# Kernel tuning notes

Hardware: AMD Instinct MI355X
Metric: run time of the kernel (lower is better)

Reference implementation:

```python
import jax, jax.numpy as jnp
import numpy as np

B, S, E, H = 2, 2048, 1024, 16
D = E // H  # head_dim = 64
SCALE = 1.0 / np.sqrt(D)


def setup_inputs() -> dict:
    key = jax.random.key(0)
    ks = jax.random.split(key, 5)
    std = 0.02
    return {
        "x": jax.random.normal(ks[0], (B, S, E), dtype=jnp.float32),
        "wq": jax.random.normal(ks[1], (E, E), dtype=jnp.float32) * std,
        "wk": jax.random.normal(ks[2], (E, E), dtype=jnp.float32) * std,
        "wv": jax.random.normal(ks[3], (E, E), dtype=jnp.float32) * std,
        "wo": jax.random.normal(ks[4], (E, E), dtype=jnp.float32) * std,
    }


def reference(x, wq, wk, wv, wo):
    # Linear projections (torch Linear: y = x @ W.T); weights stored as [out, in]
    q = jnp.einsum('bse,fe->bsf', x, wq)
    k = jnp.einsum('bse,fe->bsf', x, wk)
    v = jnp.einsum('bse,fe->bsf', x, wv)
    # split heads -> [B, H, S, D]
    q = q.reshape(B, S, H, D).transpose(0, 2, 1, 3)
    k = k.reshape(B, S, H, D).transpose(0, 2, 1, 3)
    v = v.reshape(B, S, H, D).transpose(0, 2, 1, 3)
    # scaled dot-product scores [B, H, S, S]
    scores = jnp.einsum('bhqd,bhkd->bhqk', q, k) * SCALE
    # causal mask: -inf above diagonal
    causal = jnp.triu(jnp.full((S, S), -jnp.inf, dtype=scores.dtype), k=1)
    scores = scores + causal[None, None, :, :]
    attn = jax.nn.softmax(scores, axis=-1)
    # dropout p=0 -> identity
    out = jnp.einsum('bhqk,bhkd->bhqd', attn, v)
    out = out.transpose(0, 2, 1, 3).reshape(B, S, E)
    return jnp.einsum('bse,fe->bsf', out, wo)
```

## Files before the change

kernel.cpp:

```cpp
#include <hip/hip_runtime.h>
#include <hip/hip_bf16.h>

#define B_ 2
#define S_ 2048
#define E_ 1024
#define H_ 16
#define D_ 64
#define QKV_N 3072
#define C2_ 0.18033688011112042f

typedef __attribute__((ext_vector_type(8))) unsigned short ushort8_t;
typedef __attribute__((ext_vector_type(8))) short short8_t;
typedef __attribute__((ext_vector_type(4))) float f32x4;

__device__ __forceinline__ unsigned short f2b(float f) {
    union { float f; unsigned u; } x; x.f = f;
    unsigned r = x.u + 0x7FFFu + ((x.u >> 16) & 1u);
    return (unsigned short)(r >> 16);
}
__device__ __forceinline__ ushort2 pkbf(float a, float b) {
    union { __hip_bfloat162 h; ushort2 u; } c;
    c.h = __float22bfloat162_rn(make_float2(a, b));
    return c.u;
}
__device__ __forceinline__ void glds16(const unsigned short* g, unsigned short* l) {
    __builtin_amdgcn_global_load_lds((const __attribute__((address_space(1))) void*)g,
                                     (__attribute__((address_space(3))) void*)l, 16, 0, 0);
}

__global__ __launch_bounds__(256) void cast_all(const float* __restrict__ x,
                                                const float* __restrict__ wq,
                                                const float* __restrict__ wk,
                                                const float* __restrict__ wv,
                                                const float* __restrict__ wo,
                                                unsigned short* __restrict__ xb,
                                                unsigned short* __restrict__ wb) {
    int idx = blockIdx.x * 256 + threadIdx.x;
    const float* src; unsigned short* dst; float s = 1.f; int j;
    if (idx < 1048576) {
        src = x; dst = xb; j = idx;
    } else {
        j = idx - 1048576;
        int y = j >> 18;
        src = (y == 0) ? wq : (y == 1) ? wk : (y == 2) ? wv : wo;
        dst = wb + (size_t)y * 1048576;
        j &= 262143;
        if (y == 0) s = C2_;
    }
    float4 v = ((const float4*)src)[j];
    ushort2 lo = pkbf(v.x * s, v.y * s), hi = pkbf(v.z * s, v.w * s);
    ((ushort4*)dst)[j] = make_ushort4(lo.x, lo.y, hi.x, hi.y);
}

template <int TM, bool OUT_BF16>
__device__ __forceinline__ void gemm_bt_body(const unsigned short* __restrict__ A,
                                             const unsigned short* __restrict__ Bt,
                                             void* __restrict__ Cout,
                                             int N, int K) {
    __shared__ unsigned short As[TM * 32];
    __shared__ unsigned short Bs[128 * 32];
    const int m0 = blockIdx.y * TM;
    const int n0 = blockIdx.x * 128;
    const int tid = threadIdx.x;
    const int wave = tid >> 6;
    const int lane = tid & 63;
    const int wm = (wave >> 1) * (TM / 2);
    const int wn = (wave & 1) * 64;
    const int quad = lane >> 4;
    const int l15 = lane & 15;
    constexpr int MI = TM / 32;

    f32x4 acc[MI][4] = {};

    const int srow = lane >> 2;
    const int scb  = (lane & 3) * 8;
    const unsigned short* gB0 = Bt + (size_t)(n0 + wave * 32 + srow) * K + scb;
    const unsigned short* gB1 = gB0 + (size_t)16 * K;
    unsigned short* lB0 = Bs + wave * 1024;
    unsigned short* lB1 = lB0 + 512;
    const unsigned short* gA0;
    const unsigned short* gA1 = nullptr;
    unsigned short* lA0;
    unsigned short* lA1 = nullptr;
    if (TM == 128) {
        gA0 = A + (size_t)(m0 + wave * 32 + srow) * K + scb;
        gA1 = gA0 + (size_t)16 * K;
        lA0 = As + wave * 1024; lA1 = lA0 + 512;
    } else {
        gA0 = A + (size_t)(m0 + wave * 16 + srow) * K + scb;
        lA0 = As + wave * 512;
    }

    for (int k0 = 0; k0 < K; k0 += 32) {
        __syncthreads();
        glds16(gA0 + k0, lA0);
        if (TM == 128) glds16(gA1 + k0, lA1);
        glds16(gB0 + k0, lB0);
        glds16(gB1 + k0, lB1);
        __syncthreads();

        short8_t af[MI], bfv[4];
#pragma unroll
        for (int mi = 0; mi < MI; ++mi)
            af[mi] = *(const short8_t*)(&As[(wm + mi * 16 + l15) * 32 + quad * 8]);
#pragma unroll
        for (int ni = 0; ni < 4; ++ni)
            bfv[ni] = *(const short8_t*)(&Bs[(wn + ni * 16 + l15) * 32 + quad * 8]);
#pragma unroll
        for (int mi = 0; mi < MI; ++mi)
#pragma unroll
            for (int ni = 0; ni < 4; ++ni)
                acc[mi][ni] = __builtin_amdgcn_mfma_f32_16x16x32_bf16(
                    af[mi], bfv[ni], acc[mi][ni], 0, 0, 0);
    }

#pragma unroll
    for (int mi = 0; mi < MI; ++mi)
#pragma unroll
        for (int ni = 0; ni < 4; ++ni)
#pragma unroll
            for (int r = 0; r < 4; ++r) {
                int row = m0 + wm + mi * 16 + quad * 4 + r;
                int col = n0 + wn + ni * 16 + l15;
                float val = acc[mi][ni][r];
                if (OUT_BF16)
                    ((unsigned short*)Cout)[(size_t)row * N + col] = f2b(val);
                else
                    ((float*)Cout)[(size_t)row * N + col] = val;
            }
}

__global__ __launch_bounds__(256, 2) void gemm_qkv(const unsigned short* __restrict__ xb,
                                                   const unsigned short* __restrict__ wqkv,
                                                   unsigned short* __restrict__ qkv) {
    gemm_bt_body<128, true>(xb, wqkv, qkv, QKV_N, E_);
}

__global__ __launch_bounds__(256, 2) void gemm_out(const unsigned short* __restrict__ a,
                                                   const unsigned short* __restrict__ wob,
                                                   float* __restrict__ c) {
    gemm_bt_body<64, false>(a, wob, c, E_, E_);
}

__global__ __launch_bounds__(256) void transpose_v(const unsigned short* __restrict__ qkv,
                                                   unsigned short* __restrict__ Vt) {
    __shared__ unsigned short T[64][72];
    const int b = blockIdx.z, h = blockIdx.y, kt = blockIdx.x * 64;
    const int r = threadIdx.x >> 2;
    const int g = (threadIdx.x & 3) * 16;
    const size_t goff = (size_t)(b * S_ + kt + r) * QKV_N + 2048 + h * D_ + g;
    ushort8_t v0 = *(const ushort8_t*)(qkv + goff);
    ushort8_t v1 = *(const ushort8_t*)(qkv + goff + 8);
    *(ushort8_t*)(&T[r][g])     = v0;
    *(ushort8_t*)(&T[r][g + 8]) = v1;
    __syncthreads();
    ushort8_t o0, o1;
#pragma unroll
    for (int i = 0; i < 8; ++i) { o0[i] = T[g + i][r]; o1[i] = T[g + 8 + i][r]; }
    unsigned short* op = Vt + ((size_t)((b * H_ + h) * D_ + r)) * S_ + kt + g;
    *(ushort8_t*)(op)     = o0;
    *(ushort8_t*)(op + 8) = o1;
}

__global__ __launch_bounds__(256, 2) void attn_kernel(const unsigned short* __restrict__ QKV,
                                                      const unsigned short* __restrict__ Vtg,
                                                      unsigned short* __restrict__ O) {
    __shared__ unsigned short Ks[64 * 64];
    __shared__ unsigned short Vs[64 * 64];
    __shared__ unsigned short Ps[4][32 * 64];

    const int b = blockIdx.z, h = blockIdx.y;
    const int g_ = (blockIdx.x + blockIdx.y) & 15;
    const int qc = blockIdx.z ? (15 - g_) : g_;
    const int tid = threadIdx.x;
    const int w = tid >> 6, lane = tid & 63;
    const int quad = lane >> 4, l15 = lane & 15;
    const int lx = l15 & 7;
    const int Q0 = qc * 128 + w * 32;

    short8_t bq[2][2];
#pragma unroll
    for (int qs = 0; qs < 2; ++qs) {
        const size_t qo = (size_t)(b * S_ + Q0 + qs * 16 + l15) * QKV_N + h * D_;
        bq[qs][0] = *(const short8_t*)(QKV + qo + quad * 8);
        bq[qs][1] = *(const short8_t*)(QKV + qo + 32 + quad * 8);
    }

    f32x4 Oacc[2][4] = {};
    float lsum[2] = {0.f, 0.f};
    const int qg[2] = {Q0 + l15, Q0 + 16 + l15};

    const int fo0 = ((quad) ^ lx) * 8;
    const int fo1 = ((4 + quad) ^ lx) * 8;
    const int krow = l15 * 64;
    int pwo[4];
#pragma unroll
    for (int tm = 0; tm < 4; ++tm)
        pwo[tm] = ((tm * 2 + (quad >> 1)) ^ lx) * 8 + (quad & 1) * 4;

    const int ksr = tid & 63;
    const int kb0 = (tid >> 6) * 2;
    const int vd  = tid >> 2;
    const int vb0 = (tid & 3) * 2;
    const unsigned short* Kbase = QKV + (size_t)(b * S_) * QKV_N + 1024 + h * D_;
    const unsigned short* Vbase = Vtg + (size_t)((b * H_ + h) * D_) * S_;

    const int ntiles = 2 * qc + 2;
    for (int t = 0; t < ntiles; ++t) {
        const int kt = t * 64;
        const unsigned short* kg = Kbase + (size_t)(kt + ksr) * QKV_N + kb0 * 8;
        ushort8_t k0 = *(const ushort8_t*)(kg);
        ushort8_t k1 = *(const ushort8_t*)(kg + 8);
        const unsigned short* vp = Vbase + (size_t)vd * S_ + kt + vb0 * 8;
        ushort8_t v0 = *(const ushort8_t*)(vp);
        ushort8_t v1 = *(const ushort8_t*)(vp + 8);
        __syncthreads();
        *(ushort8_t*)(&Ks[ksr * 64 + ((kb0)     ^ (ksr & 7)) * 8]) = k0;
        *(ushort8_t*)(&Ks[ksr * 64 + ((kb0 + 1) ^ (ksr & 7)) * 8]) = k1;
        *(ushort8_t*)(&Vs[vd * 64 + ((vb0)     ^ (vd & 7)) * 8]) = v0;
        *(ushort8_t*)(&Vs[vd * 64 + ((vb0 + 1) ^ (vd & 7)) * 8]) = v1;
        __syncthreads();

        if (kt > Q0 + 31) continue;
        const bool h2 = (kt < Q0);
        const int tmmax = h2 ? 4 : 2;

        if (kt + 63 <= Q0) {
#pragma unroll
            for (int tm = 0; tm < 4; ++tm) {
                short8_t ak0 = *(const short8_t*)(&Ks[tm * 1024 + krow + fo0]);
                short8_t ak1 = *(const short8_t*)(&Ks[tm * 1024 + krow + fo1]);
#pragma unroll
                for (int qs = 0; qs < 2; ++qs) {
                    f32x4 st = {0.f, 0.f, 0.f, 0.f};
                    st = __builtin_amdgcn_mfma_f32_16x16x32_bf16(ak0, bq[qs][0], st, 0, 0, 0);
                    st = __builtin_amdgcn_mfma_f32_16x16x32_bf16(ak1, bq[qs][1], st, 0, 0, 0);
                    float p0 = exp2f(st[0]), p1 = exp2f(st[1]);
                    float p2 = exp2f(st[2]), p3 = exp2f(st[3]);
                    lsum[qs] += (p0 + p1) + (p2 + p3);
                    ushort2 a = pkbf(p0, p1), c = pkbf(p2, p3);
                    *(ushort4*)(&Ps[w][(qs * 16 + l15) * 64 + pwo[tm]]) =
                        make_ushort4(a.x, a.y, c.x, c.y);
                }
            }
        } else {
            for (int tm = 0; tm < tmmax; ++tm) {
                short8_t ak0 = *(const short8_t*)(&Ks[tm * 1024 + krow + fo0]);
                short8_t ak1 = *(const short8_t*)(&Ks[tm * 1024 + krow + fo1]);
                const int kvb = kt + tm * 16 + quad * 4;
#pragma unroll
                for (int qs = 0; qs < 2; ++qs) {
                    f32x4 st = {0.f, 0.f, 0.f, 0.f};
                    st = __builtin_amdgcn_mfma_f32_16x16x32_bf16(ak0, bq[qs][0], st, 0, 0, 0);
                    st = __builtin_amdgcn_mfma_f32_16x16x32_bf16(ak1, bq[qs][1], st, 0, 0, 0);
                    float p0 = (kvb     > qg[qs]) ? 0.f : exp2f(st[0]);
                    float p1 = (kvb + 1 > qg[qs]) ? 0.f : exp2f(st[1]);
                    float p2 = (kvb + 2 > qg[qs]) ? 0.f : exp2f(st[2]);
                    float p3 = (kvb + 3 > qg[qs]) ? 0.f : exp2f(st[3]);
                    lsum[qs] += (p0 + p1) + (p2 + p3);
                    ushort2 a = pkbf(p0, p1), c = pkbf(p2, p3);
                    *(ushort4*)(&Ps[w][(qs * 16 + l15) * 64 + pwo[tm]]) =
                        make_ushort4(a.x, a.y, c.x, c.y);
                }
            }
        }

#pragma unroll
        for (int kh = 0; kh < 2; ++kh) {
            if (kh == 1 && !h2) break;
            const int fo = kh ? fo1 : fo0;
            short8_t bv[4];
#pragma unroll
            for (int tn = 0; tn < 4; ++tn)
                bv[tn] = *(const short8_t*)(&Vs[tn * 1024 + krow + fo]);
#pragma unroll
            for (int qs = 0; qs < 2; ++qs) {
                short8_t ap = *(const short8_t*)(&Ps[w][(qs * 16 + l15) * 64 + fo]);
#pragma unroll
                for (int tn = 0; tn < 4; ++tn)
                    Oacc[qs][tn] = __builtin_amdgcn_mfma_f32_16x16x32_bf16(
                        ap, bv[tn], Oacc[qs][tn], 0, 0, 0);
            }
        }
    }

#pragma unroll
    for (int qs = 0; qs < 2; ++qs) {
        float l = lsum[qs];
        l += __shfl_xor(l, 16);
        l += __shfl_xor(l, 32);
        float inv = 1.f / l;
        float lir[4];
#pragma unroll
        for (int r = 0; r < 4; ++r)
            lir[r] = __shfl(inv, quad * 4 + r);
#pragma unroll
        for (int tn = 0; tn < 4; ++tn)
#pragma unroll
            for (int r = 0; r < 4; ++r) {
                int row = Q0 + qs * 16 + quad * 4 + r;
                O[(size_t)(b * S_ + row) * E_ + h * D_ + tn * 16 + l15] =
                    f2b(Oacc[qs][tn][r] * lir[r]);
            }
    }
}

extern "C" void kernel_launch(void* const* d_in, const int* in_sizes, int n_in,
                              void* d_out, int out_size, void* d_ws, size_t ws_size,
                              hipStream_t stream) {
    const float* x  = (const float*)d_in[0];
    const float* wq = (const float*)d_in[1];
    const float* wk = (const float*)d_in[2];
    const float* wv = (const float*)d_in[3];
    const float* wo = (const float*)d_in[4];
    float* out = (float*)d_out;

    unsigned short* ws   = (unsigned short*)d_ws;
    unsigned short* xb   = ws;
    unsigned short* wqkv = ws + 4194304;
    unsigned short* wob  = ws + 7340032;
    unsigned short* qkvb = ws + 8388608;
    unsigned short* ab   = ws + 20971520;
    unsigned short* vt   = xb;

    cast_all<<<8192, 256, 0, stream>>>(x, wq, wk, wv, wo, xb, wqkv);
    gemm_qkv<<<dim3(24, 32), 256, 0, stream>>>(xb, wqkv, qkvb);
    transpose_v<<<dim3(32, 16, 2), 256, 0, stream>>>(qkvb, vt);
    attn_kernel<<<dim3(16, 16, 2), 256, 0, stream>>>(qkvb, vt, ab);
    gemm_out<<<dim3(8, 64), 256, 0, stream>>>(ab, wob, out);
}
```

Measured before the change: 199.5 us.

## Split attention work across eight waves with sixteen query rows each

The attention kernel now launches 512 threads per block, giving each of eight waves 16 query rows instead of four waves with 32 rows. K/V tile staging is spread across the larger thread count, and partially masked 16-key subtiles above the diagonal are skipped and zeroed. This is meant to raise occupancy and latency hiding, and to waste less work on the diagonal. The cost is that each K/V tile loaded to shared memory feeds fewer MFMAs per wave. Separately, the QKV GEMM launch bound is raised to three blocks per CU, which may force register spills.

Result: faster. 191.9 us (-3.8%).

```diff
diff --git a/kernel.cpp b/kernel.cpp
--- a/kernel.cpp
+++ b/kernel.cpp
@@ -130,7 +130,7 @@
             }
 }
 
-__global__ __launch_bounds__(256, 2) void gemm_qkv(const unsigned short* __restrict__ xb,
+__global__ __launch_bounds__(256, 3) void gemm_qkv(const unsigned short* __restrict__ xb,
                                                    const unsigned short* __restrict__ wqkv,
                                                    unsigned short* __restrict__ qkv) {
     gemm_bt_body<128, true>(xb, wqkv, qkv, QKV_N, E_);
@@ -162,12 +162,12 @@
     *(ushort8_t*)(op + 8) = o1;
 }
 
-__global__ __launch_bounds__(256, 2) void attn_kernel(const unsigned short* __restrict__ QKV,
+__global__ __launch_bounds__(512, 4) void attn_kernel(const unsigned short* __restrict__ QKV,
                                                       const unsigned short* __restrict__ Vtg,
                                                       unsigned short* __restrict__ O) {
     __shared__ unsigned short Ks[64 * 64];
     __shared__ unsigned short Vs[64 * 64];
-    __shared__ unsigned short Ps[4][32 * 64];
+    __shared__ unsigned short Ps[8][16 * 64];
 
     const int b = blockIdx.z, h = blockIdx.y;
     const int g_ = (blockIdx.x + blockIdx.y) & 15;
@@ -176,19 +176,15 @@
     const int w = tid >> 6, lane = tid & 63;
     const int quad = lane >> 4, l15 = lane & 15;
     const int lx = l15 & 7;
-    const int Q0 = qc * 128 + w * 32;
-
-    short8_t bq[2][2];
-#pragma unroll
-    for (int qs = 0; qs < 2; ++qs) {
-        const size_t qo = (size_t)(b * S_ + Q0 + qs * 16 + l15) * QKV_N + h * D_;
-        bq[qs][0] = *(const short8_t*)(QKV + qo + quad * 8);
-        bq[qs][1] = *(const short8_t*)(QKV + qo + 32 + quad * 8);
-    }
-
-    f32x4 Oacc[2][4] = {};
-    float lsum[2] = {0.f, 0.f};
-    const int qg[2] = {Q0 + l15, Q0 + 16 + l15};
+    const int Q0 = qc * 128 + w * 16;
+
+    const size_t qo = (size_t)(b * S_ + Q0 + l15) * QKV_N + h * D_;
+    short8_t bq0 = *(const short8_t*)(QKV + qo + quad * 8);
+    short8_t bq1 = *(const short8_t*)(QKV + qo + 32 + quad * 8);
+
+    f32x4 Oacc[4] = {};
+    float lsum = 0.f;
+    const int qg = Q0 + l15;
 
     const int fo0 = ((quad) ^ lx) * 8;
     const int fo1 = ((4 + quad) ^ lx) * 8;
@@ -198,69 +194,58 @@
     for (int tm = 0; tm < 4; ++tm)
         pwo[tm] = ((tm * 2 + (quad >> 1)) ^ lx) * 8 + (quad & 1) * 4;
 
-    const int ksr = tid & 63;
-    const int kb0 = (tid >> 6) * 2;
-    const int vd  = tid >> 2;
-    const int vb0 = (tid & 3) * 2;
+    const int srow = tid >> 3;
+    const int scb  = tid & 7;
+    const int swz  = (scb ^ (srow & 7)) * 8;
     const unsigned short* Kbase = QKV + (size_t)(b * S_) * QKV_N + 1024 + h * D_;
     const unsigned short* Vbase = Vtg + (size_t)((b * H_ + h) * D_) * S_;
 
     const int ntiles = 2 * qc + 2;
     for (int t = 0; t < ntiles; ++t) {
         const int kt = t * 64;
-        const unsigned short* kg = Kbase + (size_t)(kt + ksr) * QKV_N + kb0 * 8;
-        ushort8_t k0 = *(const ushort8_t*)(kg);
-        ushort8_t k1 = *(const ushort8_t*)(kg + 8);
-        const unsigned short* vp = Vbase + (size_t)vd * S_ + kt + vb0 * 8;
-        ushort8_t v0 = *(const ushort8_t*)(vp);
-        ushort8_t v1 = *(const ushort8_t*)(vp + 8);
+        ushort8_t k0 = *(const ushort8_t*)(Kbase + (size_t)(kt + srow) * QKV_N + scb * 8);
+        ushort8_t v0 = *(const ushort8_t*)(Vbase + (size_t)srow * S_ + kt + scb * 8);
         __syncthreads();
-        *(ushort8_t*)(&Ks[ksr * 64 + ((kb0)     ^ (ksr & 7)) * 8]) = k0;
-        *(ushort8_t*)(&Ks[ksr * 64 + ((kb0 + 1) ^ (ksr & 7)) * 8]) = k1;
-        *(ushort8_t*)(&Vs[vd * 64 + ((vb0)     ^ (vd & 7)) * 8]) = v0;
-        *(ushort8_t*)(&Vs[vd * 64 + ((vb0 + 1) ^ (vd & 7)) * 8]) = v1;
+        *(ushort8_t*)(&Ks[srow * 64 + swz]) = k0;
+        *(ushort8_t*)(&Vs[srow * 64 + swz]) = v0;
         __syncthreads();
 
-        if (kt > Q0 + 31) continue;
-        const bool h2 = (kt < Q0);
-        const int tmmax = h2 ? 4 : 2;
+        if (kt > Q0 + 15) continue;
+        const bool h2 = (kt + 32 <= Q0 + 15);
 
         if (kt + 63 <= Q0) {
 #pragma unroll
             for (int tm = 0; tm < 4; ++tm) {
                 short8_t ak0 = *(const short8_t*)(&Ks[tm * 1024 + krow + fo0]);
                 short8_t ak1 = *(const short8_t*)(&Ks[tm * 1024 + krow + fo1]);
-#pragma unroll
-                for (int qs = 0; qs < 2; ++qs) {
-                    f32x4 st = {0.f, 0.f, 0.f, 0.f};
-                    st = __builtin_amdgcn_mfma_f32_16x16x32_bf16(ak0, bq[qs][0], st, 0, 0, 0);
-                    st = __builtin_amdgcn_mfma_f32_16x16x32_bf16(ak1, bq[qs][1], st, 0, 0, 0);
-                    float p0 = exp2f(st[0]), p1 = exp2f(st[1]);
-                    float p2 = exp2f(st[2]), p3 = exp2f(st[3]);
-                    lsum[qs] += (p0 + p1) + (p2 + p3);
-                    ushort2 a = pkbf(p0, p1), c = pkbf(p2, p3);
-                    *(ushort4*)(&Ps[w][(qs * 16 + l15) * 64 + pwo[tm]]) =
-                        make_ushort4(a.x, a.y, c.x, c.y);
-                }
+                f32x4 st = {0.f, 0.f, 0.f, 0.f};
+                st = __builtin_amdgcn_mfma_f32_16x16x32_bf16(ak0, bq0, st, 0, 0, 0);
+                st = __builtin_amdgcn_mfma_f32_16x16x32_bf16(ak1, bq1, st, 0, 0, 0);
+                float p0 = exp2f(st[0]), p1 = exp2f(st[1]);
+                float p2 = exp2f(st[2]), p3 = exp2f(st[3]);
+                lsum += (p0 + p1) + (p2 + p3);
+                ushort2 a = pkbf(p0, p1), c = pkbf(p2, p3);
+                *(ushort4*)(&Ps[w][krow + pwo[tm]]) = make_ushort4(a.x, a.y, c.x, c.y);
             }
         } else {
-            for (int tm = 0; tm < tmmax; ++tm) {
-                short8_t ak0 = *(const short8_t*)(&Ks[tm * 1024 + krow + fo0]);
-                short8_t ak1 = *(const short8_t*)(&Ks[tm * 1024 + krow + fo1]);
-                const int kvb = kt + tm * 16 + quad * 4;
-#pragma unroll
-                for (int qs = 0; qs < 2; ++qs) {
+            const int need = h2 ? 4 : 2;
+            for (int tm = 0; tm < need; ++tm) {
+                if (kt + tm * 16 <= Q0 + 15) {
+                    short8_t ak0 = *(const short8_t*)(&Ks[tm * 1024 + krow + fo0]);
+                    short8_t ak1 = *(const short8_t*)(&Ks[tm * 1024 + krow + fo1]);
                     f32x4 st = {0.f, 0.f, 0.f, 0.f};
-                    st = __builtin_amdgcn_mfma_f32_16x16x32_bf16(ak0, bq[qs][0], st, 0, 0, 0);
-                    st = __builtin_amdgcn_mfma_f32_16x16x32_bf16(ak1, bq[qs][1], st, 0, 0, 0);
-                    float p0 = (kvb     > qg[qs]) ? 0.f : exp2f(st[0]);
-                    float p1 = (kvb + 1 > qg[qs]) ? 0.f : exp2f(st[1]);
-                    float p2 = (kvb + 2 > qg[qs]) ? 0.f : exp2f(st[2]);
-                    float p3 = (kvb + 3 > qg[qs]) ? 0.f : exp2f(st[3]);
-                    lsum[qs] += (p0 + p1) + (p2 + p3);
+                    st = __builtin_amdgcn_mfma_f32_16x16x32_bf16(ak0, bq0, st, 0, 0, 0);
+                    st = __builtin_amdgcn_mfma_f32_16x16x32_bf16(ak1, bq1, st, 0, 0, 0);
+                    const int kvb = kt + tm * 16 + quad * 4;
+                    float p0 = (kvb     > qg) ? 0.f : exp2f(st[0]);
+                    float p1 = (kvb + 1 > qg) ? 0.f : exp2f(st[1]);
+                    float p2 = (kvb + 2 > qg) ? 0.f : exp2f(st[2]);
+                    float p3 = (kvb + 3 > qg) ? 0.f : exp2f(st[3]);
+                    lsum += (p0 + p1) + (p2 + p3);
                     ushort2 a = pkbf(p0, p1), c = pkbf(p2, p3);
-                    *(ushort4*)(&Ps[w][(qs * 16 + l15) * 64 + pwo[tm]]) =
-                        make_ushort4(a.x, a.y, c.x, c.y);
+                    *(ushort4*)(&Ps[w][krow + pwo[tm]]) = make_ushort4(a.x, a.y, c.x, c.y);
+                } else {
+                    *(ushort4*)(&Ps[w][krow + pwo[tm]]) = make_ushort4(0, 0, 0, 0);
                 }
             }
         }
@@ -273,36 +258,30 @@
 #pragma unroll
             for (int tn = 0; tn < 4; ++tn)
                 bv[tn] = *(const short8_t*)(&Vs[tn * 1024 + krow + fo]);
-#pragma unroll
-            for (int qs = 0; qs < 2; ++qs) {
-                short8_t ap = *(const short8_t*)(&Ps[w][(qs * 16 + l15) * 64 + fo]);
-#pragma unroll
-                for (int tn = 0; tn < 4; ++tn)
-                    Oacc[qs][tn] = __builtin_amdgcn_mfma_f32_16x16x32_bf16(
-                        ap, bv[tn], Oacc[qs][tn], 0, 0, 0);
-            }
+            short8_t ap = *(const short8_t*)(&Ps[w][krow + fo]);
+#pragma unroll
+            for (int tn = 0; tn < 4; ++tn)
+                Oacc[tn] = __builtin_amdgcn_mfma_f32_16x16x32_bf16(
+                    ap, bv[tn], Oacc[tn], 0, 0, 0);
         }
     }
 
-#pragma unroll
-    for (int qs = 0; qs < 2; ++qs) {
-        float l = lsum[qs];
-        l += __shfl_xor(l, 16);
-        l += __shfl_xor(l, 32);
-        float inv = 1.f / l;
-        float lir[4];
-#pragma unroll
-        for (int r = 0; r < 4; ++r)
-            lir[r] = __shfl(inv, quad * 4 + r);
-#pragma unroll
-        for (int tn = 0; tn < 4; ++tn)
-#pragma unroll
-            for (int r = 0; r < 4; ++r) {
-                int row = Q0 + qs * 16 + quad * 4 + r;
-                O[(size_t)(b * S_ + row) * E_ + h * D_ + tn * 16 + l15] =
-                    f2b(Oacc[qs][tn][r] * lir[r]);
-            }
-    }
+    float l = lsum;
+    l += __shfl_xor(l, 16);
+    l += __shfl_xor(l, 32);
+    float inv = 1.f / l;
+    float lir[4];
+#pragma unroll
+    for (int r = 0; r < 4; ++r)
+        lir[r] = __shfl(inv, quad * 4 + r);
+#pragma unroll
+    for (int tn = 0; tn < 4; ++tn)
+#pragma unroll
+        for (int r = 0; r < 4; ++r) {
+            int row = Q0 + quad * 4 + r;
+            O[(size_t)(b * S_ + row) * E_ + h * D_ + tn * 16 + l15] =
+                f2b(Oacc[tn][r] * lir[r]);
+        }
 }
 
 extern "C" void kernel_launch(void* const* d_in, const int* in_sizes, int n_in,
@@ -326,6 +305,6 @@
     cast_all<<<8192, 256, 0, stream>>>(x, wq, wk, wv, wo, xb, wqkv);
     gemm_qkv<<<dim3(24, 32), 256, 0, stream>>>(xb, wqkv, qkvb);
     transpose_v<<<dim3(32, 16, 2), 256, 0, stream>>>(qkvb, vt);
-    attn_kernel<<<dim3(16, 16, 2), 256, 0, stream>>>(qkvb, vt, ab);
+    attn_kernel<<<dim3(16, 16, 2), 512, 0, stream>>>(qkvb, vt, ab);
     gemm_out<<<dim3(8, 64), 256, 0, stream>>>(ab, wob, out);
 }
```

## Split-K output GEMM with atomics and pair causal chunks within attention blocks

Applied to the files above, without the earlier changes.

The output projection now uses 128-row tiles with a two-way split over K. Partial sums are accumulated with float atomicAdd into an output that is zeroed by a memset first. The attention kernel pairs a long causal query chunk with a short one inside each block, so every block does roughly the same number of KV tiles, replacing the earlier cross-block balancing. Launch-bound occupancy hints are raised for the QKV GEMM and attention kernels. This costs an extra memset, atomic traffic, and possible register spills at the higher occupancy targets.

Result: slower. 230.0 us (+15.3%).

```diff
diff --git a/kernel.cpp b/kernel.cpp
--- a/kernel.cpp
+++ b/kernel.cpp
@@ -52,11 +52,11 @@
     ((ushort4*)dst)[j] = make_ushort4(lo.x, lo.y, hi.x, hi.y);
 }
 
-template <int TM, bool OUT_BF16>
+template <int TM, int MODE>
 __device__ __forceinline__ void gemm_bt_body(const unsigned short* __restrict__ A,
                                              const unsigned short* __restrict__ Bt,
                                              void* __restrict__ Cout,
-                                             int N, int K) {
+                                             int N, int K, int kbeg, int kend) {
     __shared__ unsigned short As[TM * 32];
     __shared__ unsigned short Bs[128 * 32];
     const int m0 = blockIdx.y * TM;
@@ -91,7 +91,7 @@
         lA0 = As + wave * 512;
     }
 
-    for (int k0 = 0; k0 < K; k0 += 32) {
+    for (int k0 = kbeg; k0 < kend; k0 += 32) {
         __syncthreads();
         glds16(gA0 + k0, lA0);
         if (TM == 128) glds16(gA1 + k0, lA1);
@@ -123,23 +123,26 @@
                 int row = m0 + wm + mi * 16 + quad * 4 + r;
                 int col = n0 + wn + ni * 16 + l15;
                 float val = acc[mi][ni][r];
-                if (OUT_BF16)
+                if (MODE == 0)
                     ((unsigned short*)Cout)[(size_t)row * N + col] = f2b(val);
+                else if (MODE == 1)
+                    ((float*)Cout)[(size_t)row * N + col] = val;
                 else
-                    ((float*)Cout)[(size_t)row * N + col] = val;
-            }
-}
-
-__global__ __launch_bounds__(256, 2) void gemm_qkv(const unsigned short* __restrict__ xb,
+                    atomicAdd(&((float*)Cout)[(size_t)row * N + col], val);
+            }
+}
+
+__global__ __launch_bounds__(256, 3) void gemm_qkv(const unsigned short* __restrict__ xb,
                                                    const unsigned short* __restrict__ wqkv,
                                                    unsigned short* __restrict__ qkv) {
-    gemm_bt_body<128, true>(xb, wqkv, qkv, QKV_N, E_);
+    gemm_bt_body<128, 0>(xb, wqkv, qkv, QKV_N, E_, 0, E_);
 }
 
 __global__ __launch_bounds__(256, 2) void gemm_out(const unsigned short* __restrict__ a,
                                                    const unsigned short* __restrict__ wob,
                                                    float* __restrict__ c) {
-    gemm_bt_body<64, false>(a, wob, c, E_, E_);
+    const int kbeg = blockIdx.z * 512;
+    gemm_bt_body<128, 2>(a, wob, c, E_, E_, kbeg, kbeg + 512);
 }
 
 __global__ __launch_bounds__(256) void transpose_v(const unsigned short* __restrict__ qkv,
@@ -162,7 +165,7 @@
     *(ushort8_t*)(op + 8) = o1;
 }
 
-__global__ __launch_bounds__(256, 2) void attn_kernel(const unsigned short* __restrict__ QKV,
+__global__ __launch_bounds__(256, 4) void attn_kernel(const unsigned short* __restrict__ QKV,
                                                       const unsigned short* __restrict__ Vtg,
                                                       unsigned short* __restrict__ O) {
     __shared__ unsigned short Ks[64 * 64];
@@ -170,13 +173,13 @@
     __shared__ unsigned short Ps[4][32 * 64];
 
     const int b = blockIdx.z, h = blockIdx.y;
-    const int g_ = (blockIdx.x + blockIdx.y) & 15;
-    const int qc = blockIdx.z ? (15 - g_) : g_;
+    const int cp = blockIdx.x;
     const int tid = threadIdx.x;
     const int w = tid >> 6, lane = tid & 63;
     const int quad = lane >> 4, l15 = lane & 15;
     const int lx = l15 & 7;
-    const int Q0 = qc * 128 + w * 32;
+    const int chunk = (w < 2) ? (31 - cp) : cp;
+    const int Q0 = chunk * 64 + (w & 1) * 32;
 
     short8_t bq[2][2];
 #pragma unroll
@@ -205,7 +208,7 @@
     const unsigned short* Kbase = QKV + (size_t)(b * S_) * QKV_N + 1024 + h * D_;
     const unsigned short* Vbase = Vtg + (size_t)((b * H_ + h) * D_) * S_;
 
-    const int ntiles = 2 * qc + 2;
+    const int ntiles = 32 - cp;
     for (int t = 0; t < ntiles; ++t) {
         const int kt = t * 64;
         const unsigned short* kg = Kbase + (size_t)(kt + ksr) * QKV_N + kb0 * 8;
@@ -238,9 +241,9 @@
                     float p0 = exp2f(st[0]), p1 = exp2f(st[1]);
                     float p2 = exp2f(st[2]), p3 = exp2f(st[3]);
                     lsum[qs] += (p0 + p1) + (p2 + p3);
-                    ushort2 a = pkbf(p0, p1), c = pkbf(p2, p3);
+                    ushort2 a = pkbf(p0, p1), c2 = pkbf(p2, p3);
                     *(ushort4*)(&Ps[w][(qs * 16 + l15) * 64 + pwo[tm]]) =
-                        make_ushort4(a.x, a.y, c.x, c.y);
+                        make_ushort4(a.x, a.y, c2.x, c2.y);
                 }
             }
         } else {
@@ -258,9 +261,9 @@
                     float p2 = (kvb + 2 > qg[qs]) ? 0.f : exp2f(st[2]);
                     float p3 = (kvb + 3 > qg[qs]) ? 0.f : exp2f(st[3]);
                     lsum[qs] += (p0 + p1) + (p2 + p3);
-                    ushort2 a = pkbf(p0, p1), c = pkbf(p2, p3);
+                    ushort2 a = pkbf(p0, p1), c2 = pkbf(p2, p3);
                     *(ushort4*)(&Ps[w][(qs * 16 + l15) * 64 + pwo[tm]]) =
-                        make_ushort4(a.x, a.y, c.x, c.y);
+                        make_ushort4(a.x, a.y, c2.x, c2.y);
                 }
             }
         }
@@ -327,5 +330,6 @@
     gemm_qkv<<<dim3(24, 32), 256, 0, stream>>>(xb, wqkv, qkvb);
     transpose_v<<<dim3(32, 16, 2), 256, 0, stream>>>(qkvb, vt);
     attn_kernel<<<dim3(16, 16, 2), 256, 0, stream>>>(qkvb, vt, ab);
-    gemm_out<<<dim3(8, 64), 256, 0, stream>>>(ab, wob, out);
-}
+    hipMemsetAsync(out, 0, (size_t)out_size * sizeof(float), stream);
+    gemm_out<<<dim3(8, 32, 2), 256, 0, stream>>>(ab, wob, out);
+}
```
